# Kernel optimization log

Hardware: AMD Instinct MI355X
Metric: run time of the kernel (lower is better)

Reference implementation:

```python
import jax, jax.numpy as jnp
import numpy as np

B, N, C, T = 64, 1000, 64, 32


def setup_inputs() -> dict:
    key = jax.random.key(0)
    k = jax.random.split(key, 6)
    scale = 0.05
    return {
        "X": jax.random.normal(k[0], (B, N, C, T), dtype=jnp.float32),
        "U1": jax.random.normal(k[1], (N,), dtype=jnp.float32) * scale,
        "U2": jax.random.normal(k[2], (C, N), dtype=jnp.float32) * scale,
        "U3": jax.random.normal(k[3], (C,), dtype=jnp.float32) * scale,
        "be": jax.random.normal(k[4], (T, T), dtype=jnp.float32) * scale,
        "Ve": jax.random.normal(k[5], (T, T), dtype=jnp.float32) * scale,
    }


def reference(X, U1, U2, U3, be, Ve):
    # lhs: (X^T(0,3,2,1) @ U1) @ U2  -> (B, T, N)
    lhs = jnp.einsum('bnct,n->btc', X, U1) @ U2          # (B,T,N)
    # rhs: (X^T(0,3,1,2) @ U3)^T      -> (B, N, T)
    rhs = jnp.einsum('bnct,c->bnt', X, U3)               # (B,N,T)
    # scores: (B,T,T) + be
    scores = jnp.einsum('btn,bns->bts', lhs, rhs) + be   # (B,T,T)
    E = jnp.einsum('ts,bsu->btu', Ve, jax.nn.sigmoid(scores))  # Ve @ sigmoid
    E = jax.nn.softmax(E, axis=1)                        # softmax over dim=1
    # X_hat = X @ E (broadcast over node dim): (B,N,C,T) @ (B,1,T,T)
    X_hat = jnp.einsum('bnct,bts->bncs', X, E)
    return X_hat
```

## Files before the change

### kernel.cpp

```cpp
#include <hip/hip_runtime.h>
#include <math.h>

#define BB 64
#define NN 1000
#define CC 64
#define TT 32
#define NCH 40
#define NCHUNKS 25
#define GSPLIT 8
#define GCH 125

typedef float floatx4 __attribute__((ext_vector_type(4)));

__global__ __launch_bounds__(256) void k_p1(const float* __restrict__ X,
                                            const float* __restrict__ U1,
                                            const float* __restrict__ U3,
                                            float* __restrict__ rhs,
                                            float* __restrict__ Apart) {
    int b  = blockIdx.x / NCHUNKS;
    int ch = blockIdx.x % NCHUNKS;
    int t  = threadIdx.x & 31;
    int nl = threadIdx.x >> 5;
    int n0 = ch * NCH;

    float accA[CC];
#pragma unroll
    for (int c = 0; c < CC; ++c) accA[c] = 0.f;

    for (int i = 0; i < NCH / 8; ++i) {
        int n = n0 + i * 8 + nl;
        const float* xp = X + ((size_t)(b * NN + n) * CC) * TT + t;
        float u1 = U1[n];
        float r = 0.f;
#pragma unroll
        for (int c = 0; c < CC; ++c) {
            float x = __builtin_nontemporal_load(&xp[c * TT]);
            r += U3[c] * x;
            accA[c] += u1 * x;
        }
        rhs[(size_t)(b * NN + n) * TT + t] = r;
    }

    __shared__ float buf[8][32][9];
    int t2 = threadIdx.x & 31;
    int j2 = threadIdx.x >> 5;
    for (int strip = 0; strip < 8; ++strip) {
        __syncthreads();
#pragma unroll
        for (int j = 0; j < 8; ++j) buf[nl][t][j] = accA[strip * 8 + j];
        __syncthreads();
        float v = 0.f;
#pragma unroll
        for (int k = 0; k < 8; ++k) v += buf[k][t2][j2];
        Apart[((size_t)(ch * BB + b) * TT + t2) * CC + strip * 8 + j2] = v;
    }
}

__global__ __launch_bounds__(256) void k_G(const float* __restrict__ rhs,
                                           const float* __restrict__ U2,
                                           float* __restrict__ Gpart) {
    size_t idx = (size_t)blockIdx.x * 256 + threadIdx.x;
    int within = (int)(idx & (BB * CC * TT - 1));
    int ch = (int)(idx >> 17);
    int s = within & 31;
    int c = (within >> 5) & (CC - 1);
    int b = within >> 11;
    const float* rp = rhs + (size_t)b * NN * TT + s;
    const float* up = U2 + (size_t)c * NN;
    int n0 = ch * GCH;
    float a0 = 0.f, a1 = 0.f, a2 = 0.f, a3 = 0.f, a4 = 0.f;
    for (int i = 0; i < GCH; i += 5) {
        int n = n0 + i;
        a0 += up[n + 0] * rp[(size_t)(n + 0) * TT];
        a1 += up[n + 1] * rp[(size_t)(n + 1) * TT];
        a2 += up[n + 2] * rp[(size_t)(n + 2) * TT];
        a3 += up[n + 3] * rp[(size_t)(n + 3) * TT];
        a4 += up[n + 4] * rp[(size_t)(n + 4) * TT];
    }
    Gpart[idx] = ((a0 + a1) + (a2 + a3)) + a4;
}

__global__ __launch_bounds__(1024) void k_E(const float* __restrict__ Apart,
                                            const float* __restrict__ Gpart,
                                            const float* __restrict__ be,
                                            const float* __restrict__ Ve,
                                            float* __restrict__ E) {
    int b = blockIdx.x;
    int tid = threadIdx.x;
    int u = tid & 31;
    int t = tid >> 5;
    __shared__ float As[TT][CC + 1];
    __shared__ float Gs[CC * TT];
    __shared__ float sig[TT][TT];
    __shared__ float e0[TT][TT];

    float a0 = 0.f, a1 = 0.f;
    for (int ch = 0; ch < NCHUNKS; ++ch) {
        const float* ap = Apart + ((size_t)(ch * BB + b) * TT + t) * CC;
        a0 += ap[u];
        a1 += ap[u + 32];
    }
    As[t][u] = a0;
    As[t][u + 32] = a1;

    float g0 = 0.f, g1 = 0.f;
#pragma unroll
    for (int ch = 0; ch < GSPLIT; ++ch) {
        const float* gp = Gpart + (size_t)ch * (BB * CC * TT) + (size_t)b * CC * TT;
        g0 += gp[tid];
        g1 += gp[tid + 1024];
    }
    Gs[tid] = g0;
    Gs[tid + 1024] = g1;
    __syncthreads();

    float sc = be[t * TT + u];
#pragma unroll
    for (int c = 0; c < CC; ++c) {
        sc += As[t][c] * Gs[c * TT + u];
    }
    sig[t][u] = 1.f / (1.f + __expf(-sc));
    __syncthreads();

    float e = 0.f;
#pragma unroll
    for (int s = 0; s < TT; ++s) {
        e += Ve[t * TT + s] * sig[s][u];
    }
    e0[t][u] = e;
    __syncthreads();

    float m = -1e30f;
#pragma unroll
    for (int tt = 0; tt < TT; ++tt) m = fmaxf(m, e0[tt][u]);
    float mysig = __expf(e - m);
    float sum = 0.f;
#pragma unroll
    for (int tt = 0; tt < TT; ++tt) sum += __expf(e0[tt][u] - m);
    E[((size_t)b * TT + t) * TT + u] = mysig / sum;
}

__global__ __launch_bounds__(256) void k_xhat(const float* __restrict__ X,
                                              const float* __restrict__ E,
                                              float* __restrict__ Y) {
    const int blocks_per_b = (NN * CC) / 256;
    int b = blockIdx.x / blocks_per_b;
    int tid = threadIdx.x;
    size_t qbase = (size_t)blockIdx.x * 2048;

    __shared__ floatx4 ly[256 * 8];

    const floatx4* Xq = (const floatx4*)X;
#pragma unroll
    for (int k = 0; k < 8; ++k) {
        int g = k * 256 + tid;
        int lr = g >> 3;
        int q = g & 7;
        ly[lr * 8 + (q ^ (lr & 7))] = __builtin_nontemporal_load(&Xq[qbase + g]);
    }
    __syncthreads();

    float x[TT];
#pragma unroll
    for (int j = 0; j < 8; ++j) {
        floatx4 v = ly[tid * 8 + (j ^ (tid & 7))];
        x[4 * j + 0] = v.x; x[4 * j + 1] = v.y;
        x[4 * j + 2] = v.z; x[4 * j + 3] = v.w;
    }

    const float* Eb = E + (size_t)b * TT * TT;
    float acc[TT];
#pragma unroll
    for (int s = 0; s < TT; ++s) acc[s] = 0.f;
#pragma unroll 4
    for (int t = 0; t < TT; ++t) {
        float xt = x[t];
#pragma unroll
        for (int s = 0; s < TT; ++s) {
            acc[s] += xt * Eb[t * TT + s];
        }
    }
    __syncthreads();

#pragma unroll
    for (int q = 0; q < 8; ++q) {
        floatx4 v = { acc[4 * q + 0], acc[4 * q + 1],
                      acc[4 * q + 2], acc[4 * q + 3] };
        ly[tid * 8 + (q ^ (tid & 7))] = v;
    }
    __syncthreads();

    floatx4* Yq = (floatx4*)Y;
#pragma unroll
    for (int k = 0; k < 8; ++k) {
        int g = k * 256 + tid;
        int lr = g >> 3;
        int q = g & 7;
        floatx4 v = ly[lr * 8 + (q ^ (lr & 7))];
        __builtin_nontemporal_store(v, &Yq[qbase + g]);
    }
}

extern "C" void kernel_launch(void* const* d_in, const int* in_sizes, int n_in,
                              void* d_out, int out_size, void* d_ws, size_t ws_size,
                              hipStream_t stream) {
    const float* X  = (const float*)d_in[0];
    const float* U1 = (const float*)d_in[1];
    const float* U2 = (const float*)d_in[2];
    const float* U3 = (const float*)d_in[3];
    const float* be = (const float*)d_in[4];
    const float* Ve = (const float*)d_in[5];
    float* Y = (float*)d_out;

    float* rhs   = (float*)d_ws;
    float* Apart = rhs + (size_t)BB * NN * TT;
    float* Gpart = Apart + (size_t)NCHUNKS * BB * TT * CC;
    float* E     = Gpart + (size_t)GSPLIT * BB * CC * TT;

    k_p1<<<BB * NCHUNKS, 256, 0, stream>>>(X, U1, U3, rhs, Apart);
    k_G<<<(GSPLIT * BB * CC * TT) / 256, 256, 0, stream>>>(rhs, U2, Gpart);
    k_E<<<BB, 1024, 0, stream>>>(Apart, Gpart, be, Ve, E);
    k_xhat<<<BB * ((NN * CC) / 256), 256, 0, stream>>>(X, E, Y);
}
```

Baseline: 406.4 us.

## Fuse U2 projection into first pass and load X directly in xhat

The separate k_G kernel is removed. Each k_p1 block now keeps its per-chunk rhs values in shared memory, multiplies them by a staged U2 slice and writes per-chunk G partials, which k_E sums over 25 chunks. This avoids the rhs round trip through global memory and one kernel launch, but adds shared-memory work and larger partial buffers. Separately, k_xhat now reads X rows with direct vector loads instead of staging them through swizzled LDS, which drops one barrier and the nontemporal hint on the load.

```diff
diff --git a/kernel.cpp b/kernel.cpp
--- a/kernel.cpp
+++ b/kernel.cpp
@@ -7,25 +7,34 @@
 #define TT 32
 #define NCH 40
 #define NCHUNKS 25
-#define GSPLIT 8
-#define GCH 125
 
 typedef float floatx4 __attribute__((ext_vector_type(4)));
 
 __global__ __launch_bounds__(256) void k_p1(const float* __restrict__ X,
                                             const float* __restrict__ U1,
                                             const float* __restrict__ U3,
-                                            float* __restrict__ rhs,
-                                            float* __restrict__ Apart) {
+                                            const float* __restrict__ U2,
+                                            float* __restrict__ Apart,
+                                            float* __restrict__ Gpart) {
     int b  = blockIdx.x / NCHUNKS;
     int ch = blockIdx.x % NCHUNKS;
     int t  = threadIdx.x & 31;
     int nl = threadIdx.x >> 5;
     int n0 = ch * NCH;
 
+    __shared__ float u2s[CC][NCH + 1];
+    __shared__ float rls[NCH][TT];
+    __shared__ float buf[8][32][9];
+
+    for (int k = threadIdx.x; k < CC * NCH; k += 256) {
+        int c = k / NCH, n = k % NCH;
+        u2s[c][n] = U2[(size_t)c * NN + n0 + n];
+    }
+
     float accA[CC];
 #pragma unroll
     for (int c = 0; c < CC; ++c) accA[c] = 0.f;
+    float rl[NCH / 8];
 
     for (int i = 0; i < NCH / 8; ++i) {
         int n = n0 + i * 8 + nl;
@@ -38,10 +47,36 @@
             r += U3[c] * x;
             accA[c] += u1 * x;
         }
-        rhs[(size_t)(b * NN + n) * TT + t] = r;
-    }
-
-    __shared__ float buf[8][32][9];
+        rl[i] = r;
+    }
+
+#pragma unroll
+    for (int i = 0; i < NCH / 8; ++i) rls[i * 8 + nl][t] = rl[i];
+    __syncthreads();
+
+    {
+        int c = threadIdx.x >> 2;
+        int s0 = (threadIdx.x & 3) * 8;
+        float g[8];
+#pragma unroll
+        for (int j = 0; j < 8; ++j) g[j] = 0.f;
+#pragma unroll 4
+        for (int n = 0; n < NCH; ++n) {
+            float u2v = u2s[c][n];
+            floatx4 r0 = *(const floatx4*)&rls[n][s0];
+            floatx4 r1 = *(const floatx4*)&rls[n][s0 + 4];
+            g[0] += u2v * r0.x; g[1] += u2v * r0.y;
+            g[2] += u2v * r0.z; g[3] += u2v * r0.w;
+            g[4] += u2v * r1.x; g[5] += u2v * r1.y;
+            g[6] += u2v * r1.z; g[7] += u2v * r1.w;
+        }
+        float* gp = Gpart + ((size_t)(ch * BB + b) * CC + c) * TT + s0;
+        floatx4 v0 = { g[0], g[1], g[2], g[3] };
+        floatx4 v1 = { g[4], g[5], g[6], g[7] };
+        *(floatx4*)gp = v0;
+        *(floatx4*)(gp + 4) = v1;
+    }
+
     int t2 = threadIdx.x & 31;
     int j2 = threadIdx.x >> 5;
     for (int strip = 0; strip < 8; ++strip) {
@@ -54,30 +89,6 @@
         for (int k = 0; k < 8; ++k) v += buf[k][t2][j2];
         Apart[((size_t)(ch * BB + b) * TT + t2) * CC + strip * 8 + j2] = v;
     }
-}
-
-__global__ __launch_bounds__(256) void k_G(const float* __restrict__ rhs,
-                                           const float* __restrict__ U2,
-                                           float* __restrict__ Gpart) {
-    size_t idx = (size_t)blockIdx.x * 256 + threadIdx.x;
-    int within = (int)(idx & (BB * CC * TT - 1));
-    int ch = (int)(idx >> 17);
-    int s = within & 31;
-    int c = (within >> 5) & (CC - 1);
-    int b = within >> 11;
-    const float* rp = rhs + (size_t)b * NN * TT + s;
-    const float* up = U2 + (size_t)c * NN;
-    int n0 = ch * GCH;
-    float a0 = 0.f, a1 = 0.f, a2 = 0.f, a3 = 0.f, a4 = 0.f;
-    for (int i = 0; i < GCH; i += 5) {
-        int n = n0 + i;
-        a0 += up[n + 0] * rp[(size_t)(n + 0) * TT];
-        a1 += up[n + 1] * rp[(size_t)(n + 1) * TT];
-        a2 += up[n + 2] * rp[(size_t)(n + 2) * TT];
-        a3 += up[n + 3] * rp[(size_t)(n + 3) * TT];
-        a4 += up[n + 4] * rp[(size_t)(n + 4) * TT];
-    }
-    Gpart[idx] = ((a0 + a1) + (a2 + a3)) + a4;
 }
 
 __global__ __launch_bounds__(1024) void k_E(const float* __restrict__ Apart,
@@ -104,9 +115,8 @@
     As[t][u + 32] = a1;
 
     float g0 = 0.f, g1 = 0.f;
-#pragma unroll
-    for (int ch = 0; ch < GSPLIT; ++ch) {
-        const float* gp = Gpart + (size_t)ch * (BB * CC * TT) + (size_t)b * CC * TT;
+    for (int ch = 0; ch < NCHUNKS; ++ch) {
+        const float* gp = Gpart + (size_t)(ch * BB + b) * (CC * TT);
         g0 += gp[tid];
         g1 += gp[tid + 1024];
     }
@@ -146,28 +156,15 @@
     const int blocks_per_b = (NN * CC) / 256;
     int b = blockIdx.x / blocks_per_b;
     int tid = threadIdx.x;
-    size_t qbase = (size_t)blockIdx.x * 2048;
-
-    __shared__ floatx4 ly[256 * 8];
-
-    const floatx4* Xq = (const floatx4*)X;
-#pragma unroll
-    for (int k = 0; k < 8; ++k) {
-        int g = k * 256 + tid;
-        int lr = g >> 3;
-        int q = g & 7;
-        ly[lr * 8 + (q ^ (lr & 7))] = __builtin_nontemporal_load(&Xq[qbase + g]);
-    }
-    __syncthreads();
-
+    size_t row = (size_t)blockIdx.x * 256 + tid;
+    const float* xp = X + row * TT;
     float x[TT];
 #pragma unroll
-    for (int j = 0; j < 8; ++j) {
-        floatx4 v = ly[tid * 8 + (j ^ (tid & 7))];
+    for (int j = 0; j < TT / 4; ++j) {
+        floatx4 v = *(const floatx4*)(xp + 4 * j);
         x[4 * j + 0] = v.x; x[4 * j + 1] = v.y;
         x[4 * j + 2] = v.z; x[4 * j + 3] = v.w;
     }
-
     const float* Eb = E + (size_t)b * TT * TT;
     float acc[TT];
 #pragma unroll
@@ -180,8 +177,8 @@
             acc[s] += xt * Eb[t * TT + s];
         }
     }
-    __syncthreads();
-
+
+    __shared__ floatx4 ly[256 * 8];
 #pragma unroll
     for (int q = 0; q < 8; ++q) {
         floatx4 v = { acc[4 * q + 0], acc[4 * q + 1],
@@ -191,6 +188,7 @@
     __syncthreads();
 
     floatx4* Yq = (floatx4*)Y;
+    size_t qbase = (size_t)blockIdx.x * 2048;
 #pragma unroll
     for (int k = 0; k < 8; ++k) {
         int g = k * 256 + tid;
@@ -212,13 +210,11 @@
     const float* Ve = (const float*)d_in[5];
     float* Y = (float*)d_out;
 
-    float* rhs   = (float*)d_ws;
-    float* Apart = rhs + (size_t)BB * NN * TT;
+    float* Apart = (float*)d_ws;
     float* Gpart = Apart + (size_t)NCHUNKS * BB * TT * CC;
-    float* E     = Gpart + (size_t)GSPLIT * BB * CC * TT;
-
-    k_p1<<<BB * NCHUNKS, 256, 0, stream>>>(X, U1, U3, rhs, Apart);
-    k_G<<<(GSPLIT * BB * CC * TT) / 256, 256, 0, stream>>>(rhs, U2, Gpart);
+    float* E     = Gpart + (size_t)NCHUNKS * BB * CC * TT;
+
+    k_p1<<<BB * NCHUNKS, 256, 0, stream>>>(X, U1, U3, U2, Apart, Gpart);
     k_E<<<BB, 1024, 0, stream>>>(Apart, Gpart, be, Ve, E);
     k_xhat<<<BB * ((NN * CC) / 256), 256, 0, stream>>>(X, E, Y);
 }
```

Measured after the change: 353.3 us. -13.1%, faster.
